# Kernel optimization log

Hardware: AMD Instinct MI355X
Metric: run time of the kernel (lower is better)

Reference implementation:

```python
import jax, jax.numpy as jnp
import numpy as np

N_LAYERS = 3
HIDDEN = 128
N_NODES = 50000
N_EDGES = 800000
NEG_SLOPE = 0.2  # PyG GATConv default negative_slope
EPS = 1e-16      # PyG softmax denominator eps


def setup_inputs() -> dict:
    key = jax.random.key(0)
    ks = jax.random.split(key, 6)
    z = jax.random.normal(ks[0], (N_NODES, HIDDEN), dtype=jnp.float32)
    edge_index = jax.random.randint(ks[1], (2, N_EDGES), 0, N_NODES, dtype=jnp.int32)
    scale = 1.0 / np.sqrt(HIDDEN)
    Ws = jax.random.normal(ks[2], (N_LAYERS, HIDDEN, HIDDEN), dtype=jnp.float32) * scale
    a_src = jax.random.normal(ks[3], (N_LAYERS, HIDDEN), dtype=jnp.float32) * scale
    a_dst = jax.random.normal(ks[4], (N_LAYERS, HIDDEN), dtype=jnp.float32) * scale
    bias = jnp.zeros((N_LAYERS, HIDDEN), dtype=jnp.float32)
    return {"z": z, "edge_index": edge_index, "Ws": Ws, "a_src": a_src,
            "a_dst": a_dst, "bias": bias}


def _gat_conv(h, W, a_s, a_d, b, src, dst):
    # Linear transform: [N, D]
    x = h @ W
    # Per-node attention logits, gathered per edge
    alpha_s = x @ a_s  # [N]
    alpha_d = x @ a_d  # [N]
    e = jax.nn.leaky_relu(alpha_s[src] + alpha_d[dst], NEG_SLOPE)  # [E]
    # Segment softmax over incoming edges of each destination node
    e_max = jax.ops.segment_max(e, dst, num_segments=N_NODES)
    ex = jnp.exp(e - e_max[dst])
    denom = jax.ops.segment_sum(ex, dst, num_segments=N_NODES)
    alpha = ex / (denom[dst] + EPS)  # [E]
    # Weighted scatter-aggregation of source features
    out = jax.ops.segment_sum(x[src] * alpha[:, None], dst, num_segments=N_NODES)
    return out + b


def reference(z, edge_index, Ws, a_src, a_dst, bias):
    # add_self_loops=True (PyG GATConv default)
    loop = jnp.arange(N_NODES, dtype=edge_index.dtype)
    src = jnp.concatenate([edge_index[0], loop])
    dst = jnp.concatenate([edge_index[1], loop])
    h = z
    for l in range(N_LAYERS):
        h = _gat_conv(h, Ws[l], a_src[l], a_dst[l], bias[l], src, dst)
        if l < N_LAYERS - 1:
            h = jax.nn.relu(h)
    return h
```

## Files before the change

### kernel.cpp

```cpp
#include <hip/hip_runtime.h>

#define NN 50000
#define HID 128
#define NE 800000
#define ET (NE + NN)
#define NEG_SLOPE 0.2f
#define CAP 64
#define WTOT (3 * HID * HID)
#define VTOT (3 * 3 * HID)

typedef __attribute__((ext_vector_type(8))) short short8v;
typedef __attribute__((ext_vector_type(4))) float f32x4;

__device__ inline float b2f(unsigned short u) {
    union { unsigned int i; float f; } x; x.i = ((unsigned int)u) << 16; return x.f;
}
__device__ inline unsigned short f2b(float f) {
    unsigned int x; __builtin_memcpy(&x, &f, 4);
    unsigned int lsb = (x >> 16) & 1u;
    x += 0x7fffu + lsb;
    return (unsigned short)(x >> 16);
}
__device__ inline void splitbf(float v, unsigned short& hi, unsigned short& lo) {
    hi = f2b(v);
    lo = f2b(v - b2f(hi));
}

__global__ __launch_bounds__(256) void prep(
        const unsigned short* __restrict__ z, const void* __restrict__ Ws,
        const void* __restrict__ as_, const void* __restrict__ ad_,
        const void* __restrict__ b_, unsigned short* __restrict__ Wb,
        float* __restrict__ asf, float* __restrict__ adf, float* __restrict__ bff,
        int* __restrict__ pos, int* __restrict__ flag) {
    __shared__ int sflag;
    const int t = threadIdx.x;
    if (t < 64) {
        unsigned short a = z[t * 4];
        unsigned short b = z[t * 4 + 2];
        int ea = (a >> 7) & 0xFF, eb = (b >> 7) & 0xFF;
        int w1 = (ea >= 0x9A || (ea <= 0x30 && a != 0)) ? 1 : 0;
        int w2 = (eb >= 0x9A || (eb <= 0x30 && b != 0)) ? 1 : 0;
        int wild = __popcll(__ballot(w1)) + __popcll(__ballot(w2));
        if (t == 0) sflag = (wild < 8) ? 1 : 0;
    }
    __syncthreads();
    const int f = sflag;
    const int gtid = blockIdx.x * 256 + t;
    if (gtid == 0) *flag = f;
    if (gtid < NN) pos[gtid] = 0;
    if (gtid < WTOT) {
        int L = gtid >> 14, k = (gtid >> 7) & 127, n = gtid & 127;
        float v = f ? b2f(((const unsigned short*)Ws)[gtid]) : ((const float*)Ws)[gtid];
        unsigned short hi, lo;
        splitbf(v, hi, lo);
        unsigned short* hbase = Wb + (size_t)L * 2 * HID * HID;
        unsigned short* lbase = hbase + HID * HID;
        int bo = (n * 256 + k * 2) ^ ((n & 7) << 4);
        *(unsigned short*)((char*)hbase + bo) = hi;
        lbase[n * HID + k] = lo;
    } else {
        int i = gtid - WTOT;
        if (i < VTOT) {
            int which = i / (3 * HID), j = i - which * (3 * HID);
            const void* in = which == 0 ? as_ : which == 1 ? ad_ : b_;
            float* o = which == 0 ? asf : which == 1 ? adf : bff;
            o[j] = f ? b2f(((const unsigned short*)in)[j]) : ((const float*)in)[j];
        }
    }
}

#define SCHUNK 1024
__global__ __launch_bounds__(256) void scatter_padded(
        const int* __restrict__ ei, int* __restrict__ pos, int* __restrict__ csr) {
    const int rng  = blockIdx.x & 7;
    const int base = (blockIdx.x >> 3) * SCHUNK;
#pragma unroll
    for (int k = 0; k < SCHUNK / 256; ++k) {
        int e = base + k * 256 + threadIdx.x;
        if (e >= ET) continue;
        int d = (e < NE) ? ei[NE + e] : (e - NE);
        if ((d * 8) / NN != rng) continue;
        int s = (e < NE) ? ei[e] : d;
        int slot = atomicAdd(&pos[d], 1);
        if (slot < CAP) csr[(d << 6) + slot] = s;
    }
}

__global__ __launch_bounds__(256) void gemm_alpha(
        const void* __restrict__ h_, const unsigned short* __restrict__ Wb,
        const float* __restrict__ a_s, const float* __restrict__ a_d,
        unsigned short* __restrict__ x, float* __restrict__ alpha_s, float* __restrict__ alpha_d,
        const int* __restrict__ flag) {
    __shared__ unsigned short Wh[HID * HID];
    const int t = threadIdx.x;
    const int base = blockIdx.x * 64;
    const int hf = *flag;
    const unsigned short* Wlo = Wb + HID * HID;

#pragma unroll
    for (int i = 0; i < 8; ++i) {
        int c = i * 256 + t;
        ((short8v*)Wh)[c] = ((const short8v*)Wb)[c];
    }
    __syncthreads();

    const int w  = t >> 6;
    const int l  = t & 63;
    const int lr = l & 15;
    const int lk = l >> 4;
    const int arow = base + w * 16 + lr;
    const bool rowok = (arow < NN);

    const short8v zv = (short8v){0, 0, 0, 0, 0, 0, 0, 0};
    short8v ahi[4], alo[4];
    if (hf) {
        const unsigned short* hp = (const unsigned short*)h_ + (size_t)arow * HID + lk * 8;
#pragma unroll
        for (int ks = 0; ks < 4; ++ks) {
            ahi[ks] = rowok ? *(const short8v*)(hp + ks * 32) : zv;
            alo[ks] = zv;
        }
    } else {
        const float* hp = (const float*)h_ + (size_t)arow * HID + lk * 8;
#pragma unroll
        for (int ks = 0; ks < 4; ++ks) {
            float4 v0 = make_float4(0.f, 0.f, 0.f, 0.f), v1 = v0;
            if (rowok) {
                v0 = *(const float4*)(hp + ks * 32);
                v1 = *(const float4*)(hp + ks * 32 + 4);
            }
            ushort4 h0, l0, h1, l1;
            splitbf(v0.x, h0.x, l0.x); splitbf(v0.y, h0.y, l0.y);
            splitbf(v0.z, h0.z, l0.z); splitbf(v0.w, h0.w, l0.w);
            splitbf(v1.x, h1.x, l1.x); splitbf(v1.y, h1.y, l1.y);
            splitbf(v1.z, h1.z, l1.z); splitbf(v1.w, h1.w, l1.w);
            ahi[ks] = (short8v){(short)h0.x, (short)h0.y, (short)h0.z, (short)h0.w,
                                (short)h1.x, (short)h1.y, (short)h1.z, (short)h1.w};
            alo[ks] = (short8v){(short)l0.x, (short)l0.y, (short)l0.z, (short)l0.w,
                                (short)l1.x, (short)l1.y, (short)l1.z, (short)l1.w};
        }
    }

    f32x4 acc[8];
#pragma unroll
    for (int nt = 0; nt < 8; ++nt) acc[nt] = (f32x4){0.f, 0.f, 0.f, 0.f};

    if (hf) {
#pragma unroll
        for (int ks = 0; ks < 4; ++ks) {
#pragma unroll
            for (int nt = 0; nt < 8; ++nt) {
                int row = nt * 16 + lr;
                int bo = (row * 256 + ks * 64 + lk * 16) ^ ((lr & 7) << 4);
                short8v bhi = *(const short8v*)((const char*)Wh + bo);
                short8v blo = *(const short8v*)(Wlo + row * HID + ks * 32 + lk * 8);
                acc[nt] = __builtin_amdgcn_mfma_f32_16x16x32_bf16(ahi[ks], bhi, acc[nt], 0, 0, 0);
                acc[nt] = __builtin_amdgcn_mfma_f32_16x16x32_bf16(ahi[ks], blo, acc[nt], 0, 0, 0);
            }
        }
    } else {
#pragma unroll
        for (int ks = 0; ks < 4; ++ks) {
#pragma unroll
            for (int nt = 0; nt < 8; ++nt) {
                int row = nt * 16 + lr;
                int bo = (row * 256 + ks * 64 + lk * 16) ^ ((lr & 7) << 4);
                short8v bhi = *(const short8v*)((const char*)Wh + bo);
                short8v blo = *(const short8v*)(Wlo + row * HID + ks * 32 + lk * 8);
                acc[nt] = __builtin_amdgcn_mfma_f32_16x16x32_bf16(ahi[ks], bhi, acc[nt], 0, 0, 0);
                acc[nt] = __builtin_amdgcn_mfma_f32_16x16x32_bf16(alo[ks], bhi, acc[nt], 0, 0, 0);
                acc[nt] = __builtin_amdgcn_mfma_f32_16x16x32_bf16(ahi[ks], blo, acc[nt], 0, 0, 0);
            }
        }
    }

    float ps[4] = {0.f, 0.f, 0.f, 0.f};
    float pd[4] = {0.f, 0.f, 0.f, 0.f};
#pragma unroll
    for (int nt = 0; nt < 8; ++nt) {
        float asv = a_s[nt * 16 + lr];
        float adv = a_d[nt * 16 + lr];
#pragma unroll
        for (int r = 0; r < 4; ++r) {
            ps[r] = fmaf(acc[nt][r], asv, ps[r]);
            pd[r] = fmaf(acc[nt][r], adv, pd[r]);
        }
    }
#pragma unroll
    for (int m = 8; m >= 1; m >>= 1) {
#pragma unroll
        for (int r = 0; r < 4; ++r) {
            ps[r] += __shfl_xor(ps[r], m, 16);
            pd[r] += __shfl_xor(pd[r], m, 16);
        }
    }
#pragma unroll
    for (int r = 0; r < 4; ++r) {
        int grow = base + w * 16 + lk * 4 + r;
        if (grow < NN) {
#pragma unroll
            for (int nt = 0; nt < 8; ++nt)
                x[(size_t)grow * HID + nt * 16 + lr] = f2b(acc[nt][r]);
            if (lr == 0) { alpha_s[grow] = ps[r]; alpha_d[grow] = pd[r]; }
        }
    }
}

__global__ __launch_bounds__(256) void aggregate_v3(
        const unsigned short* __restrict__ x, const int* __restrict__ deg_,
        const int* __restrict__ csr, const float* __restrict__ als,
        const float* __restrict__ ald, const float* __restrict__ bias,
        void* __restrict__ out, const int* __restrict__ flag, int do_relu) {
    const int node = (blockIdx.x * 256 + threadIdx.x) >> 6;
    const int lane = threadIdx.x & 63;
    if (node >= NN) return;
    const int deg = min(deg_[node], CAP);

    int   sidx = 0;
    float p    = 0.f;
    if (lane < deg) {
        sidx = csr[(node << 6) + lane];
        float e = als[sidx] + ald[node];
        e = fmaxf(e, NEG_SLOPE * e);
        e = fminf(e, 60.f);
        p = __expf(e);
    }
    float den = p;
#pragma unroll
    for (int m = 1; m < 64; m <<= 1) den += __shfl_xor(den, m);
    p *= 1.f / (den + 1e-16f);

    const unsigned int* x2 = (const unsigned int*)x;
    float ax = 0.f, ay = 0.f;
    for (int j0 = 0; j0 < deg; j0 += 16) {
        unsigned int u[16]; float pj[16];
#pragma unroll
        for (int k = 0; k < 16; ++k) {
            int j = j0 + k;
            int ij = __shfl(sidx, j);
            pj[k] = __shfl(p, j);
            u[k] = x2[((unsigned)ij << 6) + lane];
        }
#pragma unroll
        for (int k = 0; k < 16; ++k) {
            ax = fmaf(pj[k], b2f((unsigned short)(u[k] & 0xFFFFu)), ax);
            ay = fmaf(pj[k], b2f((unsigned short)(u[k] >> 16)), ay);
        }
    }

    float2 bv = ((const float2*)bias)[lane];
    float ox = ax + bv.x;
    float oy = ay + bv.y;
    if (do_relu) { ox = fmaxf(ox, 0.f); oy = fmaxf(oy, 0.f); }
    if (*flag) {
        ushort2 pk; pk.x = f2b(ox); pk.y = f2b(oy);
        *(ushort2*)((unsigned short*)out + (size_t)node * HID + lane * 2) = pk;
    } else {
        ((float2*)out)[(size_t)node * 64 + lane] = make_float2(ox, oy);
    }
}

extern "C" void kernel_launch(void* const* d_in, const int* in_sizes, int n_in,
                              void* d_out, int out_size, void* d_ws, size_t ws_size,
                              hipStream_t stream) {
    const void* z_in  = d_in[0];
    const int*  ei    = (const int*)d_in[1];
    const void* Ws_in = d_in[2];
    const void* as_in = d_in[3];
    const void* ad_in = d_in[4];
    const void* b_in  = d_in[5];

    char* wsp = (char*)d_ws;
    auto alloc = [&](size_t bytes) -> char* {
        char* p = wsp; wsp += (bytes + 255) & ~(size_t)255; return p;
    };
    int*            dflag   = (int*)alloc(4);
    int*            pos     = (int*)alloc(NN * 4);
    int*            csrp    = (int*)alloc((size_t)NN * CAP * 4);
    float*          alpha_s = (float*)alloc(NN * 4);
    float*          alpha_d = (float*)alloc(NN * 4);
    unsigned short* Wb      = (unsigned short*)alloc((size_t)3 * 2 * HID * HID * 2);
    float*          asf     = (float*)alloc(3 * HID * 4);
    float*          adf     = (float*)alloc(3 * HID * 4);
    float*          bff     = (float*)alloc(3 * HID * 4);
    unsigned short* xb      = (unsigned short*)alloc((size_t)NN * HID * 2);

    prep<<<197, 256, 0, stream>>>((const unsigned short*)z_in, Ws_in, as_in, ad_in, b_in,
                                  Wb, asf, adf, bff, pos, dflag);

    const int chunks = (ET + SCHUNK - 1) / SCHUNK;
    scatter_padded<<<chunks * 8, 256, 0, stream>>>(ei, pos, csrp);

    const int gemm_blocks = (NN + 63) / 64;
    const int wave_blocks = (NN + 3) / 4;
    const size_t WL = 2 * HID * HID;

    gemm_alpha<<<gemm_blocks, 256, 0, stream>>>(z_in, Wb, asf, adf, xb, alpha_s, alpha_d, dflag);
    aggregate_v3<<<wave_blocks, 256, 0, stream>>>(xb, pos, csrp, alpha_s, alpha_d, bff, d_out, dflag, 1);

    gemm_alpha<<<gemm_blocks, 256, 0, stream>>>(d_out, Wb + WL, asf + HID, adf + HID,
                                                xb, alpha_s, alpha_d, dflag);
    aggregate_v3<<<wave_blocks, 256, 0, stream>>>(xb, pos, csrp, alpha_s, alpha_d, bff + HID, d_out, dflag, 1);

    gemm_alpha<<<gemm_blocks, 256, 0, stream>>>(d_out, Wb + 2 * WL, asf + 2 * HID,
                                                adf + 2 * HID, xb, alpha_s, alpha_d, dflag);
    aggregate_v3<<<wave_blocks, 256, 0, stream>>>(xb, pos, csrp, alpha_s, alpha_d, bff + 2 * HID, d_out, dflag, 0);
}
```

Baseline: 296.7 us.

## Drop LDS weight staging and split GEMM into 2x2 warp tiles

```diff
diff --git a/kernel.cpp b/kernel.cpp
--- a/kernel.cpp
+++ b/kernel.cpp
@@ -55,8 +55,7 @@
         splitbf(v, hi, lo);
         unsigned short* hbase = Wb + (size_t)L * 2 * HID * HID;
         unsigned short* lbase = hbase + HID * HID;
-        int bo = (n * 256 + k * 2) ^ ((n & 7) << 4);
-        *(unsigned short*)((char*)hbase + bo) = hi;
+        hbase[n * HID + k] = hi;
         lbase[n * HID + k] = lo;
     } else {
         int i = gtid - WTOT;
@@ -91,119 +90,145 @@
         const float* __restrict__ a_s, const float* __restrict__ a_d,
         unsigned short* __restrict__ x, float* __restrict__ alpha_s, float* __restrict__ alpha_d,
         const int* __restrict__ flag) {
-    __shared__ unsigned short Wh[HID * HID];
+    __shared__ float aps[64], apd[64];
     const int t = threadIdx.x;
     const int base = blockIdx.x * 64;
     const int hf = *flag;
+    const unsigned short* Whi = Wb;
     const unsigned short* Wlo = Wb + HID * HID;
-
-#pragma unroll
-    for (int i = 0; i < 8; ++i) {
-        int c = i * 256 + t;
-        ((short8v*)Wh)[c] = ((const short8v*)Wb)[c];
-    }
-    __syncthreads();
 
     const int w  = t >> 6;
     const int l  = t & 63;
+    const int wr = w >> 1;
+    const int wc = w & 1;
     const int lr = l & 15;
     const int lk = l >> 4;
-    const int arow = base + w * 16 + lr;
-    const bool rowok = (arow < NN);
 
     const short8v zv = (short8v){0, 0, 0, 0, 0, 0, 0, 0};
-    short8v ahi[4], alo[4];
+    short8v ahi[2][4], alo[2][4];
+#pragma unroll
+    for (int ms = 0; ms < 2; ++ms) {
+        const int arow = base + wr * 32 + ms * 16 + lr;
+        const bool rowok = (arow < NN);
+        if (hf) {
+            const unsigned short* hp = (const unsigned short*)h_ + (size_t)arow * HID + lk * 8;
+#pragma unroll
+            for (int ks = 0; ks < 4; ++ks) {
+                ahi[ms][ks] = rowok ? *(const short8v*)(hp + ks * 32) : zv;
+                alo[ms][ks] = zv;
+            }
+        } else {
+            const float* hp = (const float*)h_ + (size_t)arow * HID + lk * 8;
+#pragma unroll
+            for (int ks = 0; ks < 4; ++ks) {
+                float4 v0 = make_float4(0.f, 0.f, 0.f, 0.f), v1 = v0;
+                if (rowok) {
+                    v0 = *(const float4*)(hp + ks * 32);
+                    v1 = *(const float4*)(hp + ks * 32 + 4);
+                }
+                ushort4 h0, l0, h1, l1;
+                splitbf(v0.x, h0.x, l0.x); splitbf(v0.y, h0.y, l0.y);
+                splitbf(v0.z, h0.z, l0.z); splitbf(v0.w, h0.w, l0.w);
+                splitbf(v1.x, h1.x, l1.x); splitbf(v1.y, h1.y, l1.y);
+                splitbf(v1.z, h1.z, l1.z); splitbf(v1.w, h1.w, l1.w);
+                ahi[ms][ks] = (short8v){(short)h0.x, (short)h0.y, (short)h0.z, (short)h0.w,
+                                        (short)h1.x, (short)h1.y, (short)h1.z, (short)h1.w};
+                alo[ms][ks] = (short8v){(short)l0.x, (short)l0.y, (short)l0.z, (short)l0.w,
+                                        (short)l1.x, (short)l1.y, (short)l1.z, (short)l1.w};
+            }
+        }
+    }
+
+    f32x4 acc[2][4];
+#pragma unroll
+    for (int ms = 0; ms < 2; ++ms)
+#pragma unroll
+        for (int nt = 0; nt < 4; ++nt) acc[ms][nt] = (f32x4){0.f, 0.f, 0.f, 0.f};
+
     if (hf) {
-        const unsigned short* hp = (const unsigned short*)h_ + (size_t)arow * HID + lk * 8;
 #pragma unroll
         for (int ks = 0; ks < 4; ++ks) {
-            ahi[ks] = rowok ? *(const short8v*)(hp + ks * 32) : zv;
-            alo[ks] = zv;
+#pragma unroll
+            for (int nt = 0; nt < 4; ++nt) {
+                int brow = wc * 64 + nt * 16 + lr;
+                short8v bhi = *(const short8v*)(Whi + brow * HID + ks * 32 + lk * 8);
+                short8v blo = *(const short8v*)(Wlo + brow * HID + ks * 32 + lk * 8);
+#pragma unroll
+                for (int ms = 0; ms < 2; ++ms) {
+                    acc[ms][nt] = __builtin_amdgcn_mfma_f32_16x16x32_bf16(ahi[ms][ks], bhi, acc[ms][nt], 0, 0, 0);
+                    acc[ms][nt] = __builtin_amdgcn_mfma_f32_16x16x32_bf16(ahi[ms][ks], blo, acc[ms][nt], 0, 0, 0);
+                }
+            }
         }
     } else {
-        const float* hp = (const float*)h_ + (size_t)arow * HID + lk * 8;
 #pragma unroll
         for (int ks = 0; ks < 4; ++ks) {
-            float4 v0 = make_float4(0.f, 0.f, 0.f, 0.f), v1 = v0;
-            if (rowok) {
-                v0 = *(const float4*)(hp + ks * 32);
-                v1 = *(const float4*)(hp + ks * 32 + 4);
-            }
-            ushort4 h0, l0, h1, l1;
-            splitbf(v0.x, h0.x, l0.x); splitbf(v0.y, h0.y, l0.y);
-            splitbf(v0.z, h0.z, l0.z); splitbf(v0.w, h0.w, l0.w);
-            splitbf(v1.x, h1.x, l1.x); splitbf(v1.y, h1.y, l1.y);
-            splitbf(v1.z, h1.z, l1.z); splitbf(v1.w, h1.w, l1.w);
-            ahi[ks] = (short8v){(short)h0.x, (short)h0.y, (short)h0.z, (short)h0.w,
-                                (short)h1.x, (short)h1.y, (short)h1.z, (short)h1.w};
-            alo[ks] = (short8v){(short)l0.x, (short)l0.y, (short)l0.z, (short)l0.w,
-                                (short)l1.x, (short)l1.y, (short)l1.z, (short)l1.w};
-        }
-    }
-
-    f32x4 acc[8];
-#pragma unroll
-    for (int nt = 0; nt < 8; ++nt) acc[nt] = (f32x4){0.f, 0.f, 0.f, 0.f};
-
-    if (hf) {
-#pragma unroll
-        for (int ks = 0; ks < 4; ++ks) {
-#pragma unroll
-            for (int nt = 0; nt < 8; ++nt) {
-                int row = nt * 16 + lr;
-                int bo = (row * 256 + ks * 64 + lk * 16) ^ ((lr & 7) << 4);
-                short8v bhi = *(const short8v*)((const char*)Wh + bo);
-                short8v blo = *(const short8v*)(Wlo + row * HID + ks * 32 + lk * 8);
-                acc[nt] = __builtin_amdgcn_mfma_f32_16x16x32_bf16(ahi[ks], bhi, acc[nt], 0, 0, 0);
-                acc[nt] = __builtin_amdgcn_mfma_f32_16x16x32_bf16(ahi[ks], blo, acc[nt], 0, 0, 0);
-            }
-        }
-    } else {
-#pragma unroll
-        for (int ks = 0; ks < 4; ++ks) {
-#pragma unroll
-            for (int nt = 0; nt < 8; ++nt) {
-                int row = nt * 16 + lr;
-                int bo = (row * 256 + ks * 64 + lk * 16) ^ ((lr & 7) << 4);
-                short8v bhi = *(const short8v*)((const char*)Wh + bo);
-                short8v blo = *(const short8v*)(Wlo + row * HID + ks * 32 + lk * 8);
-                acc[nt] = __builtin_amdgcn_mfma_f32_16x16x32_bf16(ahi[ks], bhi, acc[nt], 0, 0, 0);
-                acc[nt] = __builtin_amdgcn_mfma_f32_16x16x32_bf16(alo[ks], bhi, acc[nt], 0, 0, 0);
-                acc[nt] = __builtin_amdgcn_mfma_f32_16x16x32_bf16(ahi[ks], blo, acc[nt], 0, 0, 0);
-            }
-        }
-    }
-
-    float ps[4] = {0.f, 0.f, 0.f, 0.f};
-    float pd[4] = {0.f, 0.f, 0.f, 0.f};
-#pragma unroll
-    for (int nt = 0; nt < 8; ++nt) {
-        float asv = a_s[nt * 16 + lr];
-        float adv = a_d[nt * 16 + lr];
+#pragma unroll
+            for (int nt = 0; nt < 4; ++nt) {
+                int brow = wc * 64 + nt * 16 + lr;
+                short8v bhi = *(const short8v*)(Whi + brow * HID + ks * 32 + lk * 8);
+                short8v blo = *(const short8v*)(Wlo + brow * HID + ks * 32 + lk * 8);
+#pragma unroll
+                for (int ms = 0; ms < 2; ++ms) {
+                    acc[ms][nt] = __builtin_amdgcn_mfma_f32_16x16x32_bf16(ahi[ms][ks], bhi, acc[ms][nt], 0, 0, 0);
+                    acc[ms][nt] = __builtin_amdgcn_mfma_f32_16x16x32_bf16(alo[ms][ks], bhi, acc[ms][nt], 0, 0, 0);
+                    acc[ms][nt] = __builtin_amdgcn_mfma_f32_16x16x32_bf16(ahi[ms][ks], blo, acc[ms][nt], 0, 0, 0);
+                }
+            }
+        }
+    }
+
+    float ps[2][4] = {{0.f,0.f,0.f,0.f},{0.f,0.f,0.f,0.f}};
+    float pd[2][4] = {{0.f,0.f,0.f,0.f},{0.f,0.f,0.f,0.f}};
+#pragma unroll
+    for (int nt = 0; nt < 4; ++nt) {
+        float asv = a_s[wc * 64 + nt * 16 + lr];
+        float adv = a_d[wc * 64 + nt * 16 + lr];
+#pragma unroll
+        for (int ms = 0; ms < 2; ++ms)
+#pragma unroll
+            for (int r = 0; r < 4; ++r) {
+                ps[ms][r] = fmaf(acc[ms][nt][r], asv, ps[ms][r]);
+                pd[ms][r] = fmaf(acc[ms][nt][r], adv, pd[ms][r]);
+            }
+    }
+#pragma unroll
+    for (int m = 8; m >= 1; m >>= 1)
+#pragma unroll
+        for (int ms = 0; ms < 2; ++ms)
+#pragma unroll
+            for (int r = 0; r < 4; ++r) {
+                ps[ms][r] += __shfl_xor(ps[ms][r], m, 16);
+                pd[ms][r] += __shfl_xor(pd[ms][r], m, 16);
+            }
+    if (wc == 1 && lr == 0) {
+#pragma unroll
+        for (int ms = 0; ms < 2; ++ms)
+#pragma unroll
+            for (int r = 0; r < 4; ++r) {
+                int rib = wr * 32 + ms * 16 + lk * 4 + r;
+                aps[rib] = ps[ms][r];
+                apd[rib] = pd[ms][r];
+            }
+    }
+    __syncthreads();
+
+#pragma unroll
+    for (int ms = 0; ms < 2; ++ms)
 #pragma unroll
         for (int r = 0; r < 4; ++r) {
-            ps[r] = fmaf(acc[nt][r], asv, ps[r]);
-            pd[r] = fmaf(acc[nt][r], adv, pd[r]);
-        }
-    }
-#pragma unroll
-    for (int m = 8; m >= 1; m >>= 1) {
-#pragma unroll
-        for (int r = 0; r < 4; ++r) {
-            ps[r] += __shfl_xor(ps[r], m, 16);
-            pd[r] += __shfl_xor(pd[r], m, 16);
-        }
-    }
-#pragma unroll
-    for (int r = 0; r < 4; ++r) {
-        int grow = base + w * 16 + lk * 4 + r;
-        if (grow < NN) {
-#pragma unroll
-            for (int nt = 0; nt < 8; ++nt)
-                x[(size_t)grow * HID + nt * 16 + lr] = f2b(acc[nt][r]);
-            if (lr == 0) { alpha_s[grow] = ps[r]; alpha_d[grow] = pd[r]; }
-        }
-    }
+            int rib = wr * 32 + ms * 16 + lk * 4 + r;
+            int grow = base + rib;
+            if (grow < NN) {
+#pragma unroll
+                for (int nt = 0; nt < 4; ++nt)
+                    x[(size_t)grow * HID + wc * 64 + nt * 16 + lr] = f2b(acc[ms][nt][r]);
+                if (wc == 0 && lr == 0) {
+                    alpha_s[grow] = ps[ms][r] + aps[rib];
+                    alpha_d[grow] = pd[ms][r] + apd[rib];
+                }
+            }
+        }
 }
 
 __global__ __launch_bounds__(256) void aggregate_v3(
```

New measurement: 308.3 us. 1.04x slower.
